# Performance work log

Measured on AMD Instinct MI355X. Metric: run time of the kernel, lower is better.

## Reference

```python
import jax, jax.numpy as jnp
import numpy as np

WH, WW = 8, 8            # window size
NUM_HEADS = 8
DIM = 256
B_WIN = 2048             # num_windows * batch
TOKEN_NUM = 2            # prepended tokens (rate/SNR)
N_TOK = WH * WW + TOKEN_NUM  # 66


def _relative_position_index(wh, ww):
    coords = np.stack(np.meshgrid(np.arange(wh), np.arange(ww), indexing='ij'))  # [2,wh,ww]
    flat = coords.reshape(2, -1)                                                 # [2, wh*ww]
    rel = flat[:, :, None] - flat[:, None, :]                                    # [2, M, M]
    rel = rel.transpose(1, 2, 0).astype(np.int64)
    rel[:, :, 0] += wh - 1
    rel[:, :, 1] += ww - 1
    rel[:, :, 0] *= 2 * ww - 1
    return rel.sum(-1)  # [M, M]


def setup_inputs() -> dict:
    key = jax.random.key(0)
    ks = jax.random.split(key, 6)
    x = jax.random.normal(ks[0], (B_WIN, N_TOK, DIM), dtype=jnp.float32)
    qkv_w = jax.random.normal(ks[1], (3 * DIM, DIM), dtype=jnp.float32) * 0.02
    qkv_b = jax.random.normal(ks[2], (3 * DIM,), dtype=jnp.float32) * 0.02
    rel_bias_table = jax.random.normal(ks[3], ((2 * WH - 1) * (2 * WW - 1), NUM_HEADS), dtype=jnp.float32) * 0.02
    proj_w = jax.random.normal(ks[4], (DIM, DIM), dtype=jnp.float32) * 0.02
    proj_b = jax.random.normal(ks[5], (DIM,), dtype=jnp.float32) * 0.02
    return {"x": x, "qkv_w": qkv_w, "qkv_b": qkv_b,
            "rel_bias_table": rel_bias_table, "proj_w": proj_w, "proj_b": proj_b,
            "token_num": TOKEN_NUM}


def reference(x, qkv_w, qkv_b, rel_bias_table, proj_w, proj_b, token_num):
    B_, N, C = x.shape
    H = NUM_HEADS
    hd = C // H
    scale = hd ** (-0.5)

    # QKV projection: (B, N, 3C) -> (3, B, H, N, hd)
    qkv = (x @ qkv_w.T + qkv_b).reshape(B_, N, 3, H, hd).transpose(2, 0, 3, 1, 4)
    q, k, v = qkv[0], qkv[1], qkv[2]

    attn = jnp.einsum('bhqd,bhkd->bhqk', q * scale, k)  # [B, H, N, N]

    # relative position bias gathered from table: [H, M, M], M = WH*WW
    idx = jnp.asarray(_relative_position_index(WH, WW))
    M = WH * WW
    bias = rel_bias_table[idx.reshape(-1)].reshape(M, M, H).transpose(2, 0, 1)

    # add bias only to spatial-token block (add_token=True path)
    attn = attn.at[:, :, token_num:, token_num:].add(bias[None])

    attn = jax.nn.softmax(attn, axis=-1)

    out = jnp.einsum('bhqk,bhkd->bhqd', attn, v)          # [B, H, N, hd]
    out = out.transpose(0, 2, 1, 3).reshape(B_, N, C)
    return out @ proj_w.T + proj_b
```

## Files before the change

kernel.cpp:

```cpp
#include <hip/hip_runtime.h>
#include <hip/hip_bf16.h>

typedef __attribute__((ext_vector_type(8))) short short8;
typedef __attribute__((ext_vector_type(4))) float float4v;

#define B_WIN 2048
#define NT 66
#define DIMC 256
#define NH 8
#define HD 32
#define MTOK (B_WIN * NT)

#define WS_WQKV 0
#define WS_PW   393216
#define WS_BMAT 524288
#define WS_XBF  729088
#define WS_QKV  69935104
#define WS_NEEDED 277553152ull
#define QKV_PLANE 34603008

static __device__ __forceinline__ unsigned short f2b(float f) {
    __hip_bfloat16 h = __float2bfloat16(f);
    return *reinterpret_cast<unsigned short*>(&h);
}

__global__ __launch_bounds__(256) void prep_kernel(
    const float* __restrict__ qkv_w, const float* __restrict__ pw,
    const float* __restrict__ btab, const int* __restrict__ tnp,
    unsigned short* __restrict__ wqkv_bf, unsigned short* __restrict__ pwbf,
    float* __restrict__ Bmat)
{
    int gid = blockIdx.x * 256 + threadIdx.x;
    if (gid < 768 * 256) wqkv_bf[gid] = f2b(qkv_w[gid]);
    if (gid < 256 * 256) pwbf[gid] = f2b(pw[gid]);
    if (gid < 8 * 80 * 80) {
        int h = gid / 6400, rem = gid % 6400;
        int j = rem / 80, i = rem % 80;
        int tn = *tnp;
        float v;
        if (j >= NT) v = -1e30f;
        else if (i >= NT || i < tn || j < tn) v = 0.f;
        else {
            int ri = i - tn, rj = j - tn;
            int bidx = (((ri >> 3) - (rj >> 3) + 7) * 15) + ((ri & 7) - (rj & 7) + 7);
            v = btab[bidx * NH + h];
        }
        Bmat[gid] = v;
    }
}

__global__ __launch_bounds__(256) void xconv_kernel(
    const float* __restrict__ x, unsigned short* __restrict__ xbf)
{
    const size_t n8 = (size_t)MTOK * DIMC / 8;
    size_t stride = (size_t)gridDim.x * 256;
    for (size_t i = (size_t)blockIdx.x * 256 + threadIdx.x; i < n8; i += stride) {
        size_t base = i * 8;
        float4 a = *(const float4*)(x + base);
        float4 b = *(const float4*)(x + base + 4);
        unsigned short h8[8] = { f2b(a.x), f2b(a.y), f2b(a.z), f2b(a.w),
                                 f2b(b.x), f2b(b.y), f2b(b.z), f2b(b.w) };
        *(short8*)(xbf + base) = *(short8*)h8;
    }
}

__global__ __launch_bounds__(256) void qkv_gemm_kernel(
    const unsigned short* __restrict__ xbf,
    const unsigned short* __restrict__ wqkv_bf,
    const float* __restrict__ qkv_b,
    unsigned short* __restrict__ qkvbuf)
{
    __shared__ __align__(16) char ldsA[128 * 80];
    __shared__ __align__(16) char ldsB[128 * 80];
    const int tid = threadIdx.x;
    const int l = tid & 63, w = tid >> 6;
    const int q = l >> 4, cl = l & 15;
    const int mt = blockIdx.x / 6, nb = blockIdx.x % 6;
    const unsigned arow0 = (unsigned)mt * 128;
    const int brow0 = nb * 128;
    const int wm = w >> 1, wn = w & 1;

    float4v acc[4][4];
    #pragma unroll
    for (int mi = 0; mi < 4; ++mi)
        #pragma unroll
        for (int ni = 0; ni < 4; ++ni)
            acc[mi][ni] = (float4v){0.f, 0.f, 0.f, 0.f};

    float bias4[4], scl4[4];
    int h4[4], c4[4];
    size_t sp4[4];
    #pragma unroll
    for (int ni = 0; ni < 4; ++ni) {
        int col = brow0 + wn * 64 + ni * 16 + cl;
        bias4[ni] = qkv_b[col];
        int src = col >> 8;
        scl4[ni] = (src == 0) ? 0.17677669529663687f : 1.0f;
        h4[ni] = (col >> 5) & 7;
        c4[ni] = col & 31;
        sp4[ni] = (size_t)src * QKV_PLANE;
    }

    for (int kc = 0; kc < 8; ++kc) {
        if (kc) __syncthreads();
        #pragma unroll
        for (int s = 0; s < 2; ++s) {
            int e = tid + (s << 8);
            int r = e >> 2, c = (e & 3) << 3;
            *(short8*)(ldsA + r * 80 + (c << 1)) =
                *(const short8*)(xbf + (size_t)(arow0 + r) * DIMC + (kc << 5) + c);
            *(short8*)(ldsB + r * 80 + (c << 1)) =
                *(const short8*)(wqkv_bf + (size_t)(brow0 + r) * DIMC + (kc << 5) + c);
        }
        __syncthreads();
        short8 af[4], bf[4];
        #pragma unroll
        for (int mi = 0; mi < 4; ++mi)
            af[mi] = *(const short8*)(ldsA + (wm * 64 + mi * 16 + cl) * 80 + (q << 4));
        #pragma unroll
        for (int ni = 0; ni < 4; ++ni)
            bf[ni] = *(const short8*)(ldsB + (wn * 64 + ni * 16 + cl) * 80 + (q << 4));
        #pragma unroll
        for (int mi = 0; mi < 4; ++mi)
            #pragma unroll
            for (int ni = 0; ni < 4; ++ni)
                acc[mi][ni] = __builtin_amdgcn_mfma_f32_16x16x32_bf16(
                    af[mi], bf[ni], acc[mi][ni], 0, 0, 0);
    }

    #pragma unroll
    for (int mi = 0; mi < 4; ++mi) {
        #pragma unroll
        for (int r = 0; r < 4; ++r) {
            unsigned row = arow0 + wm * 64 + mi * 16 + (q << 2) + r;
            unsigned bb = row / 66u;
            unsigned m = row - bb * 66u;
            size_t rb = (size_t)bb * 8;
            #pragma unroll
            for (int ni = 0; ni < 4; ++ni) {
                float val = (acc[mi][ni][r] + bias4[ni]) * scl4[ni];
                qkvbuf[sp4[ni] + ((rb + h4[ni]) * 66 + m) * 32 + c4[ni]] = f2b(val);
            }
        }
    }
}

#define AC_QH 0
#define AC_KH 5280
#define AC_VT 10560
#define AC_P  17216
#define AC_SZ 33856

__global__ __launch_bounds__(256, 4) void attn_core_kernel(
    const unsigned short* __restrict__ qkvbuf,
    const float* __restrict__ Bmat,
    unsigned short* __restrict__ ybuf)
{
    __shared__ __align__(16) char pool[AC_SZ];
    __shared__ float rowsum[80];

    const int tid = threadIdx.x;
    const int l = tid & 63, w = tid >> 6;
    const int q = l >> 4, cl = l & 15;
    const int b = blockIdx.x >> 3, h = blockIdx.x & 7;
    const size_t head = (size_t)(b * 8 + h) * (NT * HD);
    const unsigned short* qsrc = qkvbuf + head;
    const unsigned short* ksrc = qsrc + (size_t)QKV_PLANE;
    const unsigned short* vsrc = ksrc + (size_t)QKV_PLANE;

    for (int i = tid; i < 32 * 104 / 2; i += 256)
        ((unsigned int*)(pool + AC_VT))[i] = 0u;
    for (int i = tid; i < 640; i += 256) {
        int m = i >> 3, j = i & 7;
        *(unsigned int*)(pool + AC_P + m * 208 + 160 + j * 4) = 0u;
    }
    if (tid < 80) rowsum[tid] = 0.f;

    for (int i = tid; i < 528; i += 256) {
        int sel = (i >= 264);
        int j = sel ? i - 264 : i;
        int r = j >> 2, c8 = (j & 3) << 3;
        const unsigned short* s = (sel ? ksrc : qsrc) + r * 32 + c8;
        *(short8*)(pool + (sel ? AC_KH : AC_QH) + r * 80 + (c8 << 1)) =
            *(const short8*)s;
    }
    for (int i = tid; i < NT * 32; i += 256) {
        int m = i >> 5, c = i & 31;
        *(unsigned short*)(pool + AC_VT + c * 208 + (m << 1)) = vsrc[i];
    }
    __syncthreads();

    for (int t = w; t < 25; t += 4) {
        int mt = t / 5, jt = t % 5;
        int am = min(mt * 16 + cl, NT - 1);
        int bj = min(jt * 16 + cl, NT - 1);
        short8 a = *(const short8*)(pool + AC_QH + am * 80 + (q << 4));
        short8 bb = *(const short8*)(pool + AC_KH + bj * 80 + (q << 4));
        float4v s = __builtin_amdgcn_mfma_f32_16x16x32_bf16(
            a, bb, (float4v){0.f, 0.f, 0.f, 0.f}, 0, 0, 0);
        int col = jt * 16 + cl;
        float4 bv = *(const float4*)(Bmat + ((h * 80 + col) * 80) + mt * 16 + (q << 2));
        float rs[4];
        #pragma unroll
        for (int r = 0; r < 4; ++r) {
            int row = mt * 16 + (q << 2) + r;
            float p = __expf(s[r] + ((const float*)&bv)[r]);
            *(unsigned short*)(pool + AC_P + row * 208 + col * 2) = f2b(p);
            rs[r] = p;
        }
        #pragma unroll
        for (int off = 1; off < 16; off <<= 1) {
            #pragma unroll
            for (int r = 0; r < 4; ++r) rs[r] += __shfl_xor(rs[r], off, 64);
        }
        if (cl == 0) {
            #pragma unroll
            for (int r = 0; r < 4; ++r)
                atomicAdd(&rowsum[mt * 16 + (q << 2) + r], rs[r]);
        }
    }
    __syncthreads();

    const int npv = (w < 2) ? 3 : 2;
    for (int i = 0; i < npv; ++i) {
        int t = w + 4 * i, mt = t % 5, nt = t / 5;
        float4v a4 = (float4v){0.f, 0.f, 0.f, 0.f};
        #pragma unroll
        for (int ks = 0; ks < 3; ++ks) {
            short8 a = *(const short8*)(pool + AC_P + (mt * 16 + cl) * 208 + (ks << 6) + (q << 4));
            short8 bb = *(const short8*)(pool + AC_VT + (nt * 16 + cl) * 208 + (ks << 6) + (q << 4));
            a4 = __builtin_amdgcn_mfma_f32_16x16x32_bf16(a, bb, a4, 0, 0, 0);
        }
        #pragma unroll
        for (int r = 0; r < 4; ++r) {
            int m = mt * 16 + (q << 2) + r;
            if (m < NT) {
                float inv = 1.f / rowsum[m];
                ybuf[(size_t)b * (NT * DIMC) + m * DIMC + (h << 5) + nt * 16 + cl] =
                    f2b(a4[r] * inv);
            }
        }
    }
}

#define OFF_XB   0
#define OFF_WBUF 34848
#define OFF_QH   45088
#define OFF_KH   50368
#define OFF_VT   55648
#define POOL_SZ  62304
#define OFF_P    0

__global__ __launch_bounds__(256, 2) void attn_fused_kernel(
    const float* __restrict__ x,
    const unsigned short* __restrict__ wqkv_bf,
    const float* __restrict__ qkv_b,
    const float* __restrict__ Bmat,
    unsigned short* __restrict__ ybuf)
{
    __shared__ __align__(16) char pool[POOL_SZ];
    __shared__ float rowsum[80];

    const int tid = threadIdx.x;
    const int l = tid & 63, w = tid >> 6;
    const int q = l >> 4, cl = l & 15;
    const int b = blockIdx.x >> 3, h = blockIdx.x & 7;
    const size_t xbase = (size_t)b * (NT * DIMC);

    for (int i = tid; i < 32 * 104 / 2; i += 256)
        ((unsigned int*)(pool + OFF_VT))[i] = 0u;
    for (int i = tid; i < NT * 64; i += 256) {
        int m = i >> 6, c4 = (i & 63) << 2;
        float4 xv = *(const float4*)(x + xbase + m * DIMC + c4);
        unsigned short h4[4] = { f2b(xv.x), f2b(xv.y), f2b(xv.z), f2b(xv.w) };
        *(ulonglong1*)(pool + OFF_XB + m * 528 + c4 * 2) = *(ulonglong1*)h4;
    }
    __syncthreads();

    const int ntiles = (w < 2) ? 8 : 7;
    float4v acc[8];
    #pragma unroll
    for (int i = 0; i < 8; ++i) acc[i] = (float4v){0.f, 0.f, 0.f, 0.f};

    for (int kc = 0; kc < 8; ++kc) {
        for (int i = tid; i < 768; i += 256) {
            int r = i >> 3, c4 = (i & 7) << 2;
            int grow = ((r >> 5) << 8) + (h << 5) + (r & 31);
            *(ulonglong1*)(pool + OFF_WBUF + r * 80 + c4 * 2) =
                *(const ulonglong1*)(wqkv_bf + grow * DIMC + (kc << 5) + c4);
        }
        __syncthreads();
        for (int i = 0; i < ntiles; ++i) {
            int t = w + 4 * i, mt = t % 5, nt = t / 5;
            int am = min(mt * 16 + cl, NT - 1);
            short8 a = *(const short8*)(pool + OFF_XB + am * 528 + (kc << 6) + (q << 4));
            short8 bb = *(const short8*)(pool + OFF_WBUF + (nt * 16 + cl) * 80 + (q << 4));
            acc[i] = __builtin_amdgcn_mfma_f32_16x16x32_bf16(a, bb, acc[i], 0, 0, 0);
        }
        __syncthreads();
    }

    for (int i = 0; i < ntiles; ++i) {
        int t = w + 4 * i, mt = t % 5, nt = t / 5;
        int ng = nt * 16 + cl;
        int src = ng >> 5, cn = ng & 31;
        float bias = qkv_b[(src << 8) + (h << 5) + cn];
        #pragma unroll
        for (int r = 0; r < 4; ++r) {
            int m = mt * 16 + (q << 2) + r;
            if (m < NT) {
                float v = acc[i][r] + bias;
                if (src == 0)
                    *(unsigned short*)(pool + OFF_QH + m * 80 + cn * 2) =
                        f2b(v * 0.17677669529663687f);
                else if (src == 1)
                    *(unsigned short*)(pool + OFF_KH + m * 80 + cn * 2) = f2b(v);
                else
                    *(unsigned short*)(pool + OFF_VT + cn * 208 + m * 2) = f2b(v);
            }
        }
    }
    __syncthreads();

    for (int i = tid; i < 80; i += 256) rowsum[i] = 0.f;
    for (int i = tid; i < 320; i += 256) {
        int m = i >> 2, c4 = 80 + ((i & 3) << 2);
        unsigned short z4[4] = {0, 0, 0, 0};
        *(ulonglong1*)(pool + OFF_P + m * 208 + c4 * 2) = *(ulonglong1*)z4;
    }
    __syncthreads();

    for (int t = w; t < 25; t += 4) {
        int mt = t / 5, jt = t % 5;
        int am = min(mt * 16 + cl, NT - 1);
        int bj = min(jt * 16 + cl, NT - 1);
        short8 a = *(const short8*)(pool + OFF_QH + am * 80 + (q << 4));
        short8 bb = *(const short8*)(pool + OFF_KH + bj * 80 + (q << 4));
        float4v s = __builtin_amdgcn_mfma_f32_16x16x32_bf16(
            a, bb, (float4v){0.f, 0.f, 0.f, 0.f}, 0, 0, 0);
        int col = jt * 16 + cl;
        float4 bv = *(const float4*)(Bmat + ((h * 80 + col) * 80) + mt * 16 + (q << 2));
        float rs[4];
        #pragma unroll
        for (int r = 0; r < 4; ++r) {
            int row = mt * 16 + (q << 2) + r;
            float p = __expf(s[r] + ((const float*)&bv)[r]);
            *(unsigned short*)(pool + OFF_P + row * 208 + col * 2) = f2b(p);
            rs[r] = p;
        }
        #pragma unroll
        for (int off = 1; off < 16; off <<= 1) {
            #pragma unroll
            for (int r = 0; r < 4; ++r) rs[r] += __shfl_xor(rs[r], off, 64);
        }
        if (cl == 0) {
            #pragma unroll
            for (int r = 0; r < 4; ++r)
                atomicAdd(&rowsum[mt * 16 + (q << 2) + r], rs[r]);
        }
    }
    __syncthreads();

    const int npv = (w < 2) ? 3 : 2;
    for (int i = 0; i < npv; ++i) {
        int t = w + 4 * i, mt = t % 5, nt = t / 5;
        float4v a4 = (float4v){0.f, 0.f, 0.f, 0.f};
        #pragma unroll
        for (int ks = 0; ks < 3; ++ks) {
            short8 a = *(const short8*)(pool + OFF_P + (mt * 16 + cl) * 208 + (ks << 6) + (q << 4));
            short8 bb = *(const short8*)(pool + OFF_VT + (nt * 16 + cl) * 208 + (ks << 6) + (q << 4));
            a4 = __builtin_amdgcn_mfma_f32_16x16x32_bf16(a, bb, a4, 0, 0, 0);
        }
        #pragma unroll
        for (int r = 0; r < 4; ++r) {
            int m = mt * 16 + (q << 2) + r;
            if (m < NT) {
                float inv = 1.f / rowsum[m];
                ybuf[xbase + m * DIMC + (h << 5) + nt * 16 + cl] = f2b(a4[r] * inv);
            }
        }
    }
}

__global__ __launch_bounds__(256) void proj_kernel(
    const unsigned short* __restrict__ ybuf,
    const unsigned short* __restrict__ pwbf,
    const float* __restrict__ pb,
    float* __restrict__ out)
{
    __shared__ __align__(16) char ldsA[128 * 80];
    __shared__ __align__(16) char ldsB[128 * 80];
    const int tid = threadIdx.x;
    const int l = tid & 63, w = tid >> 6;
    const int q = l >> 4, cl = l & 15;
    const int nb = blockIdx.x & 1;
    const size_t arow0 = (size_t)(blockIdx.x >> 1) * 128;
    const int brow0 = nb * 128;
    const int wm = w >> 1, wn = w & 1;

    float4v acc[4][4];
    #pragma unroll
    for (int mi = 0; mi < 4; ++mi)
        #pragma unroll
        for (int ni = 0; ni < 4; ++ni)
            acc[mi][ni] = (float4v){0.f, 0.f, 0.f, 0.f};

    float pbv[4];
    #pragma unroll
    for (int ni = 0; ni < 4; ++ni)
        pbv[ni] = pb[brow0 + wn * 64 + ni * 16 + cl];

    for (int kc = 0; kc < 8; ++kc) {
        if (kc) __syncthreads();
        #pragma unroll
        for (int s = 0; s < 2; ++s) {
            int e = tid + (s << 8);
            int r = e >> 2, c = (e & 3) << 3;
            *(short8*)(ldsA + r * 80 + (c << 1)) =
                *(const short8*)(ybuf + (arow0 + r) * DIMC + (kc << 5) + c);
            *(short8*)(ldsB + r * 80 + (c << 1)) =
                *(const short8*)(pwbf + (size_t)(brow0 + r) * DIMC + (kc << 5) + c);
        }
        __syncthreads();
        short8 af[4], bf[4];
        #pragma unroll
        for (int mi = 0; mi < 4; ++mi)
            af[mi] = *(const short8*)(ldsA + (wm * 64 + mi * 16 + cl) * 80 + (q << 4));
        #pragma unroll
        for (int ni = 0; ni < 4; ++ni)
            bf[ni] = *(const short8*)(ldsB + (wn * 64 + ni * 16 + cl) * 80 + (q << 4));
        #pragma unroll
        for (int mi = 0; mi < 4; ++mi)
            #pragma unroll
            for (int ni = 0; ni < 4; ++ni)
                acc[mi][ni] = __builtin_amdgcn_mfma_f32_16x16x32_bf16(
                    af[mi], bf[ni], acc[mi][ni], 0, 0, 0);
    }

    #pragma unroll
    for (int mi = 0; mi < 4; ++mi) {
        #pragma unroll
        for (int ni = 0; ni < 4; ++ni) {
            int col = brow0 + wn * 64 + ni * 16 + cl;
            #pragma unroll
            for (int r = 0; r < 4; ++r) {
                size_t row = arow0 + wm * 64 + mi * 16 + (q << 2) + r;
                out[row * DIMC + col] = acc[mi][ni][r] + pbv[ni];
            }
        }
    }
}

extern "C" void kernel_launch(void* const* d_in, const int* in_sizes, int n_in,
                              void* d_out, int out_size, void* d_ws, size_t ws_size,
                              hipStream_t stream) {
    const float* x     = (const float*)d_in[0];
    const float* qkv_w = (const float*)d_in[1];
    const float* qkv_b = (const float*)d_in[2];
    const float* btab  = (const float*)d_in[3];
    const float* pw    = (const float*)d_in[4];
    const float* pb    = (const float*)d_in[5];
    const int*   tnp   = (const int*)d_in[6];
    float* out = (float*)d_out;

    unsigned short* wqkv_bf = (unsigned short*)((char*)d_ws + WS_WQKV);
    unsigned short* pwbf    = (unsigned short*)((char*)d_ws + WS_PW);
    float*          Bmat    = (float*)((char*)d_ws + WS_BMAT);
    unsigned short* xbf     = (unsigned short*)((char*)d_ws + WS_XBF);
    unsigned short* ybuf    = (unsigned short*)((char*)d_ws + WS_XBF);
    unsigned short* qkvbuf  = (unsigned short*)((char*)d_ws + WS_QKV);

    prep_kernel<<<768, 256, 0, stream>>>(qkv_w, pw, btab, tnp, wqkv_bf, pwbf, Bmat);

    if (ws_size >= WS_NEEDED) {
        xconv_kernel<<<4096, 256, 0, stream>>>(x, xbf);
        qkv_gemm_kernel<<<(MTOK / 128) * 6, 256, 0, stream>>>(xbf, wqkv_bf, qkv_b, qkvbuf);
        attn_core_kernel<<<B_WIN * NH, 256, 0, stream>>>(qkvbuf, Bmat, ybuf);
    } else {
        attn_fused_kernel<<<B_WIN * NH, 256, 0, stream>>>(x, wqkv_bf, qkv_b, Bmat, ybuf);
    }
    proj_kernel<<<(MTOK / 128) * 2, 256, 0, stream>>>(ybuf, pwbf, pb, out);
}
```

Before: 627.4 us.

## Fuse x conversion into prep, compute softmax rowsum via ones-column MFMA, use exp2

```diff
diff --git a/kernel.cpp b/kernel.cpp
--- a/kernel.cpp
+++ b/kernel.cpp
@@ -19,6 +19,8 @@
 #define WS_NEEDED 277553152ull
 #define QKV_PLANE 34603008
 
+#define LOG2E 1.4426950408889634f
+
 static __device__ __forceinline__ unsigned short f2b(float f) {
     __hip_bfloat16 h = __float2bfloat16(f);
     return *reinterpret_cast<unsigned short*>(&h);
@@ -27,8 +29,9 @@
 __global__ __launch_bounds__(256) void prep_kernel(
     const float* __restrict__ qkv_w, const float* __restrict__ pw,
     const float* __restrict__ btab, const int* __restrict__ tnp,
+    const float* __restrict__ x,
     unsigned short* __restrict__ wqkv_bf, unsigned short* __restrict__ pwbf,
-    float* __restrict__ Bmat)
+    float* __restrict__ Bmat, unsigned short* __restrict__ xbf)
 {
     int gid = blockIdx.x * 256 + threadIdx.x;
     if (gid < 768 * 256) wqkv_bf[gid] = f2b(qkv_w[gid]);
@@ -45,16 +48,11 @@
             int bidx = (((ri >> 3) - (rj >> 3) + 7) * 15) + ((ri & 7) - (rj & 7) + 7);
             v = btab[bidx * NH + h];
         }
-        Bmat[gid] = v;
-    }
-}
-
-__global__ __launch_bounds__(256) void xconv_kernel(
-    const float* __restrict__ x, unsigned short* __restrict__ xbf)
-{
+        Bmat[gid] = v * LOG2E;
+    }
     const size_t n8 = (size_t)MTOK * DIMC / 8;
     size_t stride = (size_t)gridDim.x * 256;
-    for (size_t i = (size_t)blockIdx.x * 256 + threadIdx.x; i < n8; i += stride) {
+    for (size_t i = (size_t)gid; i < n8; i += stride) {
         size_t base = i * 8;
         float4 a = *(const float4*)(x + base);
         float4 b = *(const float4*)(x + base + 4);
@@ -95,7 +93,7 @@
         int col = brow0 + wn * 64 + ni * 16 + cl;
         bias4[ni] = qkv_b[col];
         int src = col >> 8;
-        scl4[ni] = (src == 0) ? 0.17677669529663687f : 1.0f;
+        scl4[ni] = (src == 0) ? (0.17677669529663687f * LOG2E) : 1.0f;
         h4[ni] = (col >> 5) & 7;
         c4[ni] = col & 31;
         sp4[ni] = (size_t)src * QKV_PLANE;
@@ -148,8 +146,8 @@
 #define AC_QH 0
 #define AC_KH 5280
 #define AC_VT 10560
-#define AC_P  17216
-#define AC_SZ 33856
+#define AC_P  20544
+#define AC_SZ 37184
 
 __global__ __launch_bounds__(256, 4) void attn_core_kernel(
     const unsigned short* __restrict__ qkvbuf,
@@ -168,76 +166,103 @@
     const unsigned short* ksrc = qsrc + (size_t)QKV_PLANE;
     const unsigned short* vsrc = ksrc + (size_t)QKV_PLANE;
 
-    for (int i = tid; i < 32 * 104 / 2; i += 256)
-        ((unsigned int*)(pool + AC_VT))[i] = 0u;
+    short8 rq0 = *(const short8*)(qsrc + (size_t)tid * 8);
+    short8 rk0 = *(const short8*)(ksrc + (size_t)tid * 8);
+    short8 rv0 = *(const short8*)(vsrc + (size_t)tid * 8);
+    short8 rq1, rk1, rv1;
+    if (tid < 8) {
+        rq1 = *(const short8*)(qsrc + (size_t)(256 + tid) * 8);
+        rk1 = *(const short8*)(ksrc + (size_t)(256 + tid) * 8);
+        rv1 = *(const short8*)(vsrc + (size_t)(256 + tid) * 8);
+    }
+
+    #pragma unroll
+    for (int s = 0; s < 2; ++s) {
+        int i = tid + (s << 8);
+        int row = i >> 4, j = i & 15;
+        *(unsigned int*)(pool + AC_VT + row * 208 + 132 + j * 4) = 0u;
+    }
+    if (tid < 48)
+        *(unsigned int*)(pool + AC_VT + 32 * 208 + tid * 4) = 0x3F803F80u;
     for (int i = tid; i < 640; i += 256) {
         int m = i >> 3, j = i & 7;
         *(unsigned int*)(pool + AC_P + m * 208 + 160 + j * 4) = 0u;
     }
-    if (tid < 80) rowsum[tid] = 0.f;
-
-    for (int i = tid; i < 528; i += 256) {
-        int sel = (i >= 264);
-        int j = sel ? i - 264 : i;
-        int r = j >> 2, c8 = (j & 3) << 3;
-        const unsigned short* s = (sel ? ksrc : qsrc) + r * 32 + c8;
-        *(short8*)(pool + (sel ? AC_KH : AC_QH) + r * 80 + (c8 << 1)) =
-            *(const short8*)s;
-    }
-    for (int i = tid; i < NT * 32; i += 256) {
-        int m = i >> 5, c = i & 31;
-        *(unsigned short*)(pool + AC_VT + c * 208 + (m << 1)) = vsrc[i];
+
+    {
+        int r = tid >> 2, c8 = (tid & 3) << 3;
+        *(short8*)(pool + AC_QH + r * 80 + (c8 << 1)) = rq0;
+        *(short8*)(pool + AC_KH + r * 80 + (c8 << 1)) = rk0;
+        #pragma unroll
+        for (int e = 0; e < 8; ++e)
+            *(unsigned short*)(pool + AC_VT + (c8 + e) * 208 + (r << 1)) =
+                ((unsigned short*)&rv0)[e];
+        if (tid < 8) {
+            int r1 = 64 + (tid >> 2), c81 = (tid & 3) << 3;
+            *(short8*)(pool + AC_QH + r1 * 80 + (c81 << 1)) = rq1;
+            *(short8*)(pool + AC_KH + r1 * 80 + (c81 << 1)) = rk1;
+            #pragma unroll
+            for (int e = 0; e < 8; ++e)
+                *(unsigned short*)(pool + AC_VT + (c81 + e) * 208 + (r1 << 1)) =
+                    ((unsigned short*)&rv1)[e];
+        }
     }
     __syncthreads();
 
     for (int t = w; t < 25; t += 4) {
-        int mt = t / 5, jt = t % 5;
-        int am = min(mt * 16 + cl, NT - 1);
-        int bj = min(jt * 16 + cl, NT - 1);
-        short8 a = *(const short8*)(pool + AC_QH + am * 80 + (q << 4));
-        short8 bb = *(const short8*)(pool + AC_KH + bj * 80 + (q << 4));
+        int mt = t / 5, jt = t - mt * 5;
+        short8 a = *(const short8*)(pool + AC_QH + (mt * 16 + cl) * 80 + (q << 4));
+        short8 bb = *(const short8*)(pool + AC_KH + (jt * 16 + cl) * 80 + (q << 4));
         float4v s = __builtin_amdgcn_mfma_f32_16x16x32_bf16(
             a, bb, (float4v){0.f, 0.f, 0.f, 0.f}, 0, 0, 0);
         int col = jt * 16 + cl;
         float4 bv = *(const float4*)(Bmat + ((h * 80 + col) * 80) + mt * 16 + (q << 2));
-        float rs[4];
         #pragma unroll
         for (int r = 0; r < 4; ++r) {
-            int row = mt * 16 + (q << 2) + r;
-            float p = __expf(s[r] + ((const float*)&bv)[r]);
-            *(unsigned short*)(pool + AC_P + row * 208 + col * 2) = f2b(p);
-            rs[r] = p;
-        }
-        #pragma unroll
-        for (int off = 1; off < 16; off <<= 1) {
-            #pragma unroll
-            for (int r = 0; r < 4; ++r) rs[r] += __shfl_xor(rs[r], off, 64);
-        }
-        if (cl == 0) {
-            #pragma unroll
-            for (int r = 0; r < 4; ++r)
-                atomicAdd(&rowsum[mt * 16 + (q << 2) + r], rs[r]);
-        }
-    }
-    __syncthreads();
-
-    const int npv = (w < 2) ? 3 : 2;
-    for (int i = 0; i < npv; ++i) {
-        int t = w + 4 * i, mt = t % 5, nt = t / 5;
-        float4v a4 = (float4v){0.f, 0.f, 0.f, 0.f};
-        #pragma unroll
-        for (int ks = 0; ks < 3; ++ks) {
-            short8 a = *(const short8*)(pool + AC_P + (mt * 16 + cl) * 208 + (ks << 6) + (q << 4));
-            short8 bb = *(const short8*)(pool + AC_VT + (nt * 16 + cl) * 208 + (ks << 6) + (q << 4));
-            a4 = __builtin_amdgcn_mfma_f32_16x16x32_bf16(a, bb, a4, 0, 0, 0);
-        }
-        #pragma unroll
-        for (int r = 0; r < 4; ++r) {
-            int m = mt * 16 + (q << 2) + r;
-            if (m < NT) {
-                float inv = 1.f / rowsum[m];
-                ybuf[(size_t)b * (NT * DIMC) + m * DIMC + (h << 5) + nt * 16 + cl] =
-                    f2b(a4[r] * inv);
+            float p = exp2f(s[r] + ((const float*)&bv)[r]);
+            *(unsigned short*)(pool + AC_P + (mt * 16 + (q << 2) + r) * 208 + col * 2) = f2b(p);
+        }
+    }
+    __syncthreads();
+
+    float4v yac[4];
+    int mts[4], nts[4];
+    #pragma unroll
+    for (int i = 0; i < 4; ++i) {
+        int t = w + 4 * i;
+        mts[i] = -1; nts[i] = -1;
+        if (t < 15) {
+            int mt = t / 3, nt = t - mt * 3;
+            mts[i] = mt; nts[i] = nt;
+            float4v a4 = (float4v){0.f, 0.f, 0.f, 0.f};
+            #pragma unroll
+            for (int ks = 0; ks < 3; ++ks) {
+                short8 a = *(const short8*)(pool + AC_P + (mt * 16 + cl) * 208 + (ks << 6) + (q << 4));
+                short8 bb = *(const short8*)(pool + AC_VT + (nt * 16 + cl) * 208 + (ks << 6) + (q << 4));
+                a4 = __builtin_amdgcn_mfma_f32_16x16x32_bf16(a, bb, a4, 0, 0, 0);
+            }
+            yac[i] = a4;
+            if (nt == 2 && cl == 0) {
+                #pragma unroll
+                for (int r = 0; r < 4; ++r)
+                    rowsum[mt * 16 + (q << 2) + r] = a4[r];
+            }
+        }
+    }
+    __syncthreads();
+
+    #pragma unroll
+    for (int i = 0; i < 4; ++i) {
+        if (mts[i] >= 0 && nts[i] != 2) {
+            int mt = mts[i], nt = nts[i];
+            #pragma unroll
+            for (int r = 0; r < 4; ++r) {
+                int m = mt * 16 + (q << 2) + r;
+                if (m < NT) {
+                    float inv = 1.f / rowsum[m];
+                    ybuf[(size_t)b * (NT * DIMC) + m * DIMC + (h << 5) + nt * 16 + cl] =
+                        f2b(yac[i][r] * inv);
+                }
             }
         }
     }
@@ -312,7 +337,7 @@
                 float v = acc[i][r] + bias;
                 if (src == 0)
                     *(unsigned short*)(pool + OFF_QH + m * 80 + cn * 2) =
-                        f2b(v * 0.17677669529663687f);
+                        f2b(v * (0.17677669529663687f * LOG2E));
                 else if (src == 1)
                     *(unsigned short*)(pool + OFF_KH + m * 80 + cn * 2) = f2b(v);
                 else
@@ -344,7 +369,7 @@
         #pragma unroll
         for (int r = 0; r < 4; ++r) {
             int row = mt * 16 + (q << 2) + r;
-            float p = __expf(s[r] + ((const float*)&bv)[r]);
+            float p = exp2f(s[r] + ((const float*)&bv)[r]);
             *(unsigned short*)(pool + OFF_P + row * 208 + col * 2) = f2b(p);
             rs[r] = p;
         }
@@ -470,10 +495,10 @@
     unsigned short* ybuf    = (unsigned short*)((char*)d_ws + WS_XBF);
     unsigned short* qkvbuf  = (unsigned short*)((char*)d_ws + WS_QKV);
 
-    prep_kernel<<<768, 256, 0, stream>>>(qkv_w, pw, btab, tnp, wqkv_bf, pwbf, Bmat);
+    prep_kernel<<<4096, 256, 0, stream>>>(qkv_w, pw, btab, tnp, x,
+                                          wqkv_bf, pwbf, Bmat, xbf);
 
     if (ws_size >= WS_NEEDED) {
-        xconv_kernel<<<4096, 256, 0, stream>>>(x, xbf);
         qkv_gemm_kernel<<<(MTOK / 128) * 6, 256, 0, stream>>>(xbf, wqkv_bf, qkv_b, qkvbuf);
         attn_core_kernel<<<B_WIN * NH, 256, 0, stream>>>(qkvbuf, Bmat, ybuf);
     } else {
```

Result: faster. 518.4 us (-17.4%).
